# Kernel optimization log

Hardware: AMD Instinct MI355X
Metric: run time of the kernel (lower is better)

The kernel has to match this reference:

```python
import jax, jax.numpy as jnp
import numpy as np

VOCAB, EMBED, HIDDEN, CH = 500, 80, 512, 128
B, L, T = 128, 784, 256


def setup_inputs() -> dict:
    key = jax.random.key(0)
    ks = jax.random.split(key, 14)
    s = lambda fan_in: 1.0 / np.sqrt(fan_in)
    return {
        "latent_rep": jax.random.normal(ks[0], (B, L, CH), jnp.float32),
        "formulas": jax.random.randint(ks[1], (B, T), 0, VOCAB),
        "embedding": jax.random.normal(ks[2], (VOCAB, EMBED), jnp.float32),
        "W_ih": jax.random.uniform(ks[3], (4 * HIDDEN, HIDDEN + EMBED), jnp.float32, -s(HIDDEN), s(HIDDEN)),
        "b_ih": jax.random.uniform(ks[4], (4 * HIDDEN,), jnp.float32, -s(HIDDEN), s(HIDDEN)),
        "W_hh": jax.random.uniform(ks[5], (4 * HIDDEN, HIDDEN), jnp.float32, -s(HIDDEN), s(HIDDEN)),
        "b_hh": jax.random.uniform(ks[6], (4 * HIDDEN,), jnp.float32, -s(HIDDEN), s(HIDDEN)),
        "Wh": jax.random.uniform(ks[7], (HIDDEN, CH), jnp.float32, -s(CH), s(CH)),
        "bh": jax.random.uniform(ks[8], (HIDDEN,), jnp.float32, -s(CH), s(CH)),
        "Wc": jax.random.uniform(ks[9], (HIDDEN, CH), jnp.float32, -s(CH), s(CH)),
        "bc": jax.random.uniform(ks[10], (HIDDEN,), jnp.float32, -s(CH), s(CH)),
        "Wo": jax.random.uniform(ks[11], (HIDDEN, CH), jnp.float32, -s(CH), s(CH)),
        "bo": jax.random.uniform(ks[12], (HIDDEN,), jnp.float32, -s(CH), s(CH)),
    }


def reference(latent_rep, formulas, embedding, W_ih, b_ih, W_hh, b_hh, Wh, bh, Wc, bc, Wo, bo):
    # init_lstm: tanh(Linear(mean over spatial positions))
    mean_lr = latent_rep.mean(axis=1)                       # [B, C]
    h0 = jnp.tanh(mean_lr @ Wh.T + bh)                       # [B, H]
    c0 = jnp.tanh(mean_lr @ Wc.T + bc)
    o0 = jnp.tanh(mean_lr @ Wo.T + bo)                       # fixed across steps in source

    emb = embedding[formulas]                                # [B, T, E]
    xs = jnp.swapaxes(emb, 0, 1)                             # [T, B, E]

    def step(carry, emb_t):
        h, c = carry
        inp = jnp.concatenate([o0, emb_t], axis=1)           # [B, H+E]
        gates = inp @ W_ih.T + b_ih + h @ W_hh.T + b_hh      # [B, 4H]
        i_g, f_g, g_g, o_g = jnp.split(gates, 4, axis=1)
        c_new = jax.nn.sigmoid(f_g) * c + jax.nn.sigmoid(i_g) * jnp.tanh(g_g)
        h_new = jax.nn.sigmoid(o_g) * jnp.tanh(c_new)
        # dropout in eval mode = identity
        return (h_new, c_new), h_new

    _, hs = jax.lax.scan(step, (h0, c0), xs)                 # hs: [T, B, H]
    return jnp.swapaxes(hs, 0, 1)                            # [B, T, H]
```

## Files before the change

kernel.cpp:

```cpp
#include <hip/hip_runtime.h>
#include <hip/hip_bf16.h>
#include <stdint.h>

typedef unsigned int uint32;
typedef __attribute__((ext_vector_type(8))) short short8;
typedef __attribute__((ext_vector_type(4))) float f32x4;

#define NB 128
#define NT 256
#define NH 512
#define NE 80
#define NCH 128
#define NL 784
#define NV 500
#define NG4 2048

__device__ __forceinline__ unsigned short f2bf(float f){
  union { float f; unsigned int i; } v; v.f = f;
  unsigned int r = v.i + 0x7FFFu + ((v.i >> 16) & 1u);
  return (unsigned short)(r >> 16);
}
__device__ __forceinline__ float sigf(float x){ return 1.0f/(1.0f + __expf(-x)); }
__device__ __forceinline__ float tanhfast(float x){ return 1.0f - 2.0f/(__expf(2.0f*x)+1.0f); }

__global__ void k_mean(const float* __restrict__ lat, float* __restrict__ meanv){
  int b = blockIdx.x;
  int tid = threadIdx.x;
  int c4 = tid & 31;
  int part = tid >> 5;
  const float4* row = (const float4*)(lat + (size_t)b*NL*NCH);
  float sx=0.f, sy=0.f, sz=0.f, sw=0.f;
  for (int l=part; l<NL; l+=8){
    float4 v = row[l*32 + c4];
    sx+=v.x; sy+=v.y; sz+=v.z; sw+=v.w;
  }
  __shared__ float red[8][32][4];
  red[part][c4][0]=sx; red[part][c4][1]=sy; red[part][c4][2]=sz; red[part][c4][3]=sw;
  __syncthreads();
  if (part==0){
    float a0=0,a1=0,a2=0,a3=0;
    #pragma unroll
    for (int p=0;p<8;p++){ a0+=red[p][c4][0]; a1+=red[p][c4][1]; a2+=red[p][c4][2]; a3+=red[p][c4][3]; }
    float4 o; o.x=a0*(1.0f/NL); o.y=a1*(1.0f/NL); o.z=a2*(1.0f/NL); o.w=a3*(1.0f/NL);
    ((float4*)meanv)[b*32 + c4] = o;
  }
}

__global__ void k_init(const float* __restrict__ meanv,
    const float* __restrict__ Wh, const float* __restrict__ bh,
    const float* __restrict__ Wc, const float* __restrict__ bc,
    const float* __restrict__ Wo, const float* __restrict__ bo,
    float* __restrict__ c0, float* __restrict__ o0, unsigned short* __restrict__ hbuf0){
  int b = blockIdx.x; int j = threadIdx.x;
  const float* m = meanv + b*NCH;
  const float4* wh = (const float4*)(Wh + (size_t)j*NCH);
  const float4* wc = (const float4*)(Wc + (size_t)j*NCH);
  const float4* wo = (const float4*)(Wo + (size_t)j*NCH);
  float sh=0.f, sc=0.f, so=0.f;
  for (int c=0; c<NCH/4; c++){
    float4 vh = wh[c], vc = wc[c], vo = wo[c];
    float m0=m[c*4], m1=m[c*4+1], m2=m[c*4+2], m3=m[c*4+3];
    sh += m0*vh.x + m1*vh.y + m2*vh.z + m3*vh.w;
    sc += m0*vc.x + m1*vc.y + m2*vc.z + m3*vc.w;
    so += m0*vo.x + m1*vo.y + m2*vo.z + m3*vo.w;
  }
  float h0 = tanhf(sh + bh[j]);
  c0[b*NH+j] = tanhf(sc + bc[j]);
  o0[b*NH+j] = tanhf(so + bo[j]);
  hbuf0[b*NH+j] = f2bf(h0);
}

__global__ void k_table(const float* __restrict__ emb,
                        const float* __restrict__ Wih,
                        float* __restrict__ table){
  int v = blockIdx.x;
  int n = blockIdx.y*256 + threadIdx.x;
  const float4* wr = (const float4*)(Wih + (size_t)n*(NH+NE) + NH);
  const float4* er = (const float4*)(emb + v*NE);
  float s = 0.f;
  for (int e4=0; e4<NE/4; e4++){
    float4 w = wr[e4], e = er[e4];
    s += w.x*e.x + w.y*e.y + w.z*e.z + w.w*e.w;
  }
  table[(size_t)v*NG4 + n] = s;
}

__global__ void k_base(const float* __restrict__ o0,
                       const float* __restrict__ Wih,
                       const float* __restrict__ bih,
                       const float* __restrict__ bhh,
                       float* __restrict__ base){
  int b = blockIdx.x;
  int n = blockIdx.y*256 + threadIdx.x;
  const float4* o = (const float4*)(o0 + b*NH);
  const float4* wr = (const float4*)(Wih + (size_t)n*(NH+NE));
  float s = bih[n] + bhh[n];
  for (int k4=0;k4<NH/4;k4++){
    float4 w = wr[k4], v = o[k4];
    s += w.x*v.x + w.y*v.y + w.z*v.z + w.w*v.w;
  }
  base[(size_t)b*NG4 + n] = s;
}

#define HBUF_U (NB*(NH/2))

__global__ __launch_bounds__(256, 1) void k_lstm(
    const float* __restrict__ Whh,
    const int* __restrict__ formulas,
    const float* __restrict__ table,
    const float* __restrict__ base,
    const float* __restrict__ c0,
    uint32* hbuf, int* flags,
    float* __restrict__ out)
{
  int bid = blockIdx.x;
  int g = bid & 7, s = bid >> 3;
  int tid = threadIdx.x;
  int lane = tid & 63, w = tid >> 6;
  int b0 = g*16, u0 = s*32;

  __shared__ __align__(16) char h_lds[16*1024];
  __shared__ float G[16*132 + 4];

  short8 bw[2][16];
  {
    int krow = (lane >> 4) * 8;
    #pragma unroll
    for (int h2=0; h2<2; h2++){
      int c_loc = w*32 + h2*16 + (lane & 15);
      int wrow = (c_loc >> 5)*NH + u0 + (c_loc & 31);
      const float4* p4 = (const float4*)(Whh + (size_t)wrow*NH + krow);
      #pragma unroll
      for (int ks=0; ks<16; ks++){
        float4 lo = p4[ks*8], hi = p4[ks*8+1];
        short8 t;
        t[0]=(short)f2bf(lo.x); t[1]=(short)f2bf(lo.y); t[2]=(short)f2bf(lo.z); t[3]=(short)f2bf(lo.w);
        t[4]=(short)f2bf(hi.x); t[5]=(short)f2bf(hi.y); t[6]=(short)f2bf(hi.z); t[7]=(short)f2bf(hi.w);
        bw[h2][ks] = t;
      }
    }
  }

  int r_e = tid >> 4, up = tid & 15;
  int be = b0 + r_e;
  float cst0 = c0[be*NH + u0 + 2*up];
  float cst1 = c0[be*NH + u0 + 2*up + 1];

  float2 bsv[4];
  #pragma unroll
  for (int gt=0; gt<4; gt++)
    bsv[gt] = *(const float2*)(base + (size_t)be*NG4 + gt*NH + u0 + 2*up);

  float2 tbv[4];
  {
    int tok0 = formulas[be*NT + 0];
    #pragma unroll
    for (int gt=0; gt<4; gt++)
      tbv[gt] = *(const float2*)(table + (size_t)tok0*NG4 + gt*NH + u0 + 2*up);
  }

  int arow = lane & 15;
  int abyte = arow*1024 + ((lane>>4)*8)*2;
  int aswz = (arow & 7) << 4;

  int* myflag = flags + g*16 + s;
  const int* pollptr = flags + g*16 + (lane & 15);

  for (int t=0; t<NT; t++){
    const uint32* hrd = hbuf + (t & 1)*HBUF_U;
    uint32*       hwr = hbuf + ((t+1) & 1)*HBUF_U;

    if (t > 0){
      if (w == 0){
        int guard = 0;
        while (1){
          int v = __hip_atomic_load(pollptr, __ATOMIC_RELAXED, __HIP_MEMORY_SCOPE_AGENT);
          if (__all(v >= t)) break;
          __builtin_amdgcn_s_sleep(1);
          if (++guard > (1<<16)) break;
        }
      }
      __syncthreads();
    }

    uint32 vals[16];
    #pragma unroll
    for (int it=0; it<16; it++){
      int i = tid + it*256;
      int r = i >> 8, cu = i & 255;
      vals[it] = __hip_atomic_load(&hrd[(b0+r)*(NH/2) + cu],
                                   __ATOMIC_RELAXED, __HIP_MEMORY_SCOPE_AGENT);
    }
    #pragma unroll
    for (int it=0; it<16; it++){
      int i = tid + it*256;
      int r = i >> 8, cu = i & 255;
      *(uint32*)(h_lds + ((r*1024 + cu*4) ^ ((r & 7) << 4))) = vals[it];
    }
    __syncthreads();

    f32x4 acc0 = {0.f,0.f,0.f,0.f}, acc1 = {0.f,0.f,0.f,0.f};
    #pragma unroll
    for (int ks=0; ks<16; ks++){
      short8 a = *(const short8*)(h_lds + ((abyte + ks*64) ^ aswz));
      acc0 = __builtin_amdgcn_mfma_f32_16x16x32_bf16(a, bw[0][ks], acc0, 0, 0, 0);
      acc1 = __builtin_amdgcn_mfma_f32_16x16x32_bf16(a, bw[1][ks], acc1, 0, 0, 0);
    }

    {
      int rbase = (lane>>4)*4;
      int col0 = (w*2+0)*16 + (lane&15);
      int col1 = (w*2+1)*16 + (lane&15);
      #pragma unroll
      for (int r4=0;r4<4;r4++){
        G[(rbase+r4)*132 + col0] = acc0[r4];
        G[(rbase+r4)*132 + col1] = acc1[r4];
      }
    }
    __syncthreads();

    float hn0, hn1;
    {
      const float* Gr = G + r_e*132 + 2*up;
      float gi0 = Gr[0]   + tbv[0].x + bsv[0].x;
      float gi1 = Gr[1]   + tbv[0].y + bsv[0].y;
      float gf0 = Gr[32]  + tbv[1].x + bsv[1].x;
      float gf1 = Gr[33]  + tbv[1].y + bsv[1].y;
      float gg0 = Gr[64]  + tbv[2].x + bsv[2].x;
      float gg1 = Gr[65]  + tbv[2].y + bsv[2].y;
      float go0 = Gr[96]  + tbv[3].x + bsv[3].x;
      float go1 = Gr[97]  + tbv[3].y + bsv[3].y;
      float cn0 = sigf(gf0)*cst0 + sigf(gi0)*tanhfast(gg0);
      float cn1 = sigf(gf1)*cst1 + sigf(gi1)*tanhfast(gg1);
      cst0 = cn0; cst1 = cn1;
      hn0 = sigf(go0)*tanhfast(cn0);
      hn1 = sigf(go1)*tanhfast(cn1);
    }

    if (t < NT-1){
      uint32 packed = (uint32)f2bf(hn0) | ((uint32)f2bf(hn1) << 16);
      __hip_atomic_store(&hwr[be*(NH/2) + (u0/2 + up)], packed,
                         __ATOMIC_RELAXED, __HIP_MEMORY_SCOPE_AGENT);
    }
    __syncthreads();
    if (t < NT-1 && tid == 0)
      __hip_atomic_store(myflag, t+1, __ATOMIC_RELAXED, __HIP_MEMORY_SCOPE_AGENT);

    {
      float2 ov; ov.x = hn0; ov.y = hn1;
      *(float2*)(out + ((size_t)be*NT + t)*NH + u0 + 2*up) = ov;
    }
    if (t < NT-1){
      int tokn = formulas[be*NT + t + 1];
      #pragma unroll
      for (int gt=0; gt<4; gt++)
        tbv[gt] = *(const float2*)(table + (size_t)tokn*NG4 + gt*NH + u0 + 2*up);
    }
  }
}

extern "C" void kernel_launch(void* const* d_in, const int* in_sizes, int n_in,
                              void* d_out, int out_size, void* d_ws, size_t ws_size,
                              hipStream_t stream) {
  const float* lat      = (const float*)d_in[0];
  const int*   formulas = (const int*)d_in[1];
  const float* emb      = (const float*)d_in[2];
  const float* Wih      = (const float*)d_in[3];
  const float* bih      = (const float*)d_in[4];
  const float* Whh      = (const float*)d_in[5];
  const float* bhh      = (const float*)d_in[6];
  const float* Wh       = (const float*)d_in[7];
  const float* bh       = (const float*)d_in[8];
  const float* Wc       = (const float*)d_in[9];
  const float* bc       = (const float*)d_in[10];
  const float* Wo       = (const float*)d_in[11];
  const float* bo       = (const float*)d_in[12];
  float* out = (float*)d_out;

  char* ws = (char*)d_ws;
  float* meanv = (float*)ws;  ws += (size_t)NB*NCH*4;
  float* c0    = (float*)ws;  ws += (size_t)NB*NH*4;
  float* o0    = (float*)ws;  ws += (size_t)NB*NH*4;
  float* table = (float*)ws;  ws += (size_t)NV*NG4*4;
  float* base  = (float*)ws;  ws += (size_t)NB*NG4*4;
  uint32* hbuf = (uint32*)ws; ws += (size_t)2*HBUF_U*4;
  int*   flags = (int*)ws;    ws += 512;

  hipMemsetAsync(flags, 0, 512, stream);
  k_mean <<<NB, 256, 0, stream>>>(lat, meanv);
  k_init <<<NB, NH, 0, stream>>>(meanv, Wh, bh, Wc, bc, Wo, bo, c0, o0, (unsigned short*)hbuf);
  k_table<<<dim3(NV, 8), 256, 0, stream>>>(emb, Wih, table);
  k_base <<<dim3(NB, 8), 256, 0, stream>>>(o0, Wih, bih, bhh, base);
  k_lstm <<<NB, 256, 0, stream>>>(Whh, formulas, table, base, c0, hbuf, flags, out);
}
```

Before: 712.6 us.

## Fuse mean/init kernels, retile table and base GEMVs, drop LSTM poll barrier

Merges the spatial mean and LSTM-initialisation kernels into one launch. The embedding-projection table and the o0 base-gate kernels are rewritten to stage operands in LDS and reuse weights held in registers. In the recurrent kernel, every wave now polls the step flags itself, replacing the single-wave poll followed by a block barrier. These changes target launch overhead, redundant global weight reads in the precompute stage, and per-step barrier latency. The trade-off is more atomic polling traffic, and the table kernel now runs only 32 blocks.

```diff
diff --git a/kernel.cpp b/kernel.cpp
--- a/kernel.cpp
+++ b/kernel.cpp
@@ -3,6 +3,7 @@
 #include <stdint.h>
 
 typedef unsigned int uint32;
+typedef unsigned long long uint64;
 typedef __attribute__((ext_vector_type(8))) short short8;
 typedef __attribute__((ext_vector_type(4))) float f32x4;
 
@@ -15,6 +16,8 @@
 #define NV 500
 #define NG4 2048
 
+#define HBUF_U (NB*(NH/2))
+
 __device__ __forceinline__ unsigned short f2bf(float f){
   union { float f; unsigned int i; } v; v.f = f;
   unsigned int r = v.i + 0x7FFFu + ((v.i >> 16) & 1u);
@@ -23,86 +26,123 @@
 __device__ __forceinline__ float sigf(float x){ return 1.0f/(1.0f + __expf(-x)); }
 __device__ __forceinline__ float tanhfast(float x){ return 1.0f - 2.0f/(__expf(2.0f*x)+1.0f); }
 
-__global__ void k_mean(const float* __restrict__ lat, float* __restrict__ meanv){
-  int b = blockIdx.x;
-  int tid = threadIdx.x;
-  int c4 = tid & 31;
-  int part = tid >> 5;
-  const float4* row = (const float4*)(lat + (size_t)b*NL*NCH);
-  float sx=0.f, sy=0.f, sz=0.f, sw=0.f;
-  for (int l=part; l<NL; l+=8){
-    float4 v = row[l*32 + c4];
-    sx+=v.x; sy+=v.y; sz+=v.z; sw+=v.w;
-  }
-  __shared__ float red[8][32][4];
-  red[part][c4][0]=sx; red[part][c4][1]=sy; red[part][c4][2]=sz; red[part][c4][3]=sw;
-  __syncthreads();
-  if (part==0){
-    float a0=0,a1=0,a2=0,a3=0;
-    #pragma unroll
-    for (int p=0;p<8;p++){ a0+=red[p][c4][0]; a1+=red[p][c4][1]; a2+=red[p][c4][2]; a3+=red[p][c4][3]; }
-    float4 o; o.x=a0*(1.0f/NL); o.y=a1*(1.0f/NL); o.z=a2*(1.0f/NL); o.w=a3*(1.0f/NL);
-    ((float4*)meanv)[b*32 + c4] = o;
-  }
-}
-
-__global__ void k_init(const float* __restrict__ meanv,
+__global__ __launch_bounds__(512) void k_meaninit(const float* __restrict__ lat,
     const float* __restrict__ Wh, const float* __restrict__ bh,
     const float* __restrict__ Wc, const float* __restrict__ bc,
     const float* __restrict__ Wo, const float* __restrict__ bo,
-    float* __restrict__ c0, float* __restrict__ o0, unsigned short* __restrict__ hbuf0){
-  int b = blockIdx.x; int j = threadIdx.x;
-  const float* m = meanv + b*NCH;
+    float* __restrict__ c0, float* __restrict__ o0, uint32* __restrict__ hbuf0){
+  int b = blockIdx.x;
+  int tid = threadIdx.x;
+  __shared__ float red[16][32][4];
+  __shared__ float msh[128];
+  __shared__ unsigned short hsh[NH];
+
+  {
+    int c4 = tid & 31, part = tid >> 5;
+    const float4* row = (const float4*)(lat + (size_t)b*NL*NCH);
+    float sx=0.f, sy=0.f, sz=0.f, sw=0.f;
+    for (int l=part; l<NL; l+=16){
+      float4 v = row[l*32 + c4];
+      sx+=v.x; sy+=v.y; sz+=v.z; sw+=v.w;
+    }
+    red[part][c4][0]=sx; red[part][c4][1]=sy; red[part][c4][2]=sz; red[part][c4][3]=sw;
+  }
+  __syncthreads();
+  if (tid < 128){
+    int cc4 = tid >> 2, ci = tid & 3;
+    float a = 0.f;
+    #pragma unroll
+    for (int p=0;p<16;p++) a += red[p][cc4][ci];
+    msh[tid] = a * (1.0f/NL);
+  }
+  __syncthreads();
+
+  int j = tid;
   const float4* wh = (const float4*)(Wh + (size_t)j*NCH);
   const float4* wc = (const float4*)(Wc + (size_t)j*NCH);
   const float4* wo = (const float4*)(Wo + (size_t)j*NCH);
   float sh=0.f, sc=0.f, so=0.f;
+  #pragma unroll 8
   for (int c=0; c<NCH/4; c++){
     float4 vh = wh[c], vc = wc[c], vo = wo[c];
-    float m0=m[c*4], m1=m[c*4+1], m2=m[c*4+2], m3=m[c*4+3];
-    sh += m0*vh.x + m1*vh.y + m2*vh.z + m3*vh.w;
-    sc += m0*vc.x + m1*vc.y + m2*vc.z + m3*vc.w;
-    so += m0*vo.x + m1*vo.y + m2*vo.z + m3*vo.w;
+    float4 mv = *(const float4*)&msh[c*4];
+    sh += mv.x*vh.x + mv.y*vh.y + mv.z*vh.z + mv.w*vh.w;
+    sc += mv.x*vc.x + mv.y*vc.y + mv.z*vc.z + mv.w*vc.w;
+    so += mv.x*vo.x + mv.y*vo.y + mv.z*vo.z + mv.w*vo.w;
   }
   float h0 = tanhf(sh + bh[j]);
   c0[b*NH+j] = tanhf(sc + bc[j]);
   o0[b*NH+j] = tanhf(so + bo[j]);
-  hbuf0[b*NH+j] = f2bf(h0);
-}
-
-__global__ void k_table(const float* __restrict__ emb,
-                        const float* __restrict__ Wih,
-                        float* __restrict__ table){
-  int v = blockIdx.x;
-  int n = blockIdx.y*256 + threadIdx.x;
-  const float4* wr = (const float4*)(Wih + (size_t)n*(NH+NE) + NH);
-  const float4* er = (const float4*)(emb + v*NE);
-  float s = 0.f;
-  for (int e4=0; e4<NE/4; e4++){
-    float4 w = wr[e4], e = er[e4];
-    s += w.x*e.x + w.y*e.y + w.z*e.z + w.w*e.w;
-  }
-  table[(size_t)v*NG4 + n] = s;
-}
-
-__global__ void k_base(const float* __restrict__ o0,
+  hsh[j] = f2bf(h0);
+  __syncthreads();
+  if (j < NH/2)
+    hbuf0[(size_t)b*(NH/2) + j] = (uint32)hsh[2*j] | ((uint32)hsh[2*j+1] << 16);
+}
+
+__global__ __launch_bounds__(256) void k_table(const float* __restrict__ emb,
+                                               const float* __restrict__ Wih,
+                                               float* __restrict__ table){
+  int n0 = blockIdx.x * 64;
+  int tid = threadIdx.x;
+  __shared__ float el[100][84];
+  int n = tid & 63;
+  float4 wr[20];
+  {
+    const float4* wp = (const float4*)(Wih + (size_t)(n0+n)*(NH+NE) + NH);
+    #pragma unroll
+    for (int k=0;k<20;k++) wr[k] = wp[k];
+  }
+  for (int v0 = 0; v0 < NV; v0 += 100){
+    __syncthreads();
+    for (int i = tid; i < 100*20; i += 256){
+      int r = i/20, k4 = i - r*20;
+      *(float4*)&el[r][k4*4] = *(const float4*)(emb + (size_t)(v0+r)*NE + k4*4);
+    }
+    __syncthreads();
+    int vl = tid >> 6;
+    for (int v = vl; v < 100; v += 4){
+      float s = 0.f;
+      #pragma unroll
+      for (int k=0;k<20;k++){
+        float4 e = *(const float4*)&el[v][k*4];
+        s += e.x*wr[k].x + e.y*wr[k].y + e.z*wr[k].z + e.w*wr[k].w;
+      }
+      table[(size_t)(v0+v)*NG4 + n0 + n] = s;
+    }
+  }
+}
+
+__global__ __launch_bounds__(256) void k_base(const float* __restrict__ o0,
                        const float* __restrict__ Wih,
                        const float* __restrict__ bih,
                        const float* __restrict__ bhh,
                        float* __restrict__ base){
-  int b = blockIdx.x;
-  int n = blockIdx.y*256 + threadIdx.x;
-  const float4* o = (const float4*)(o0 + b*NH);
-  const float4* wr = (const float4*)(Wih + (size_t)n*(NH+NE));
-  float s = bih[n] + bhh[n];
-  for (int k4=0;k4<NH/4;k4++){
-    float4 w = wr[k4], v = o[k4];
-    s += w.x*v.x + w.y*v.y + w.z*v.z + w.w*v.w;
-  }
-  base[(size_t)b*NG4 + n] = s;
-}
-
-#define HBUF_U (NB*(NH/2))
+  int bg = blockIdx.x & 7, nc = blockIdx.x >> 3;
+  int b0 = bg*16, n0 = nc*128;
+  int tid = threadIdx.x;
+  __shared__ float ol[16][520];
+  for (int i = tid; i < 16*128; i += 256){
+    int r = i >> 7, k4 = i & 127;
+    *(float4*)&ol[r][k4*4] = *(const float4*)(o0 + (size_t)(b0+r)*NH + k4*4);
+  }
+  __syncthreads();
+  int r = tid >> 4;
+  int ni = (tid & 15)*8;
+  float acc[8];
+  #pragma unroll
+  for (int q=0;q<8;q++) acc[q] = bih[n0+ni+q] + bhh[n0+ni+q];
+  for (int k4 = 0; k4 < 128; k4++){
+    float4 ov = *(const float4*)&ol[r][k4*4];
+    #pragma unroll
+    for (int q=0;q<8;q++){
+      float4 wv = *(const float4*)(Wih + (size_t)(n0+ni+q)*(NH+NE) + k4*4);
+      acc[q] += ov.x*wv.x + ov.y*wv.y + ov.z*wv.z + ov.w*wv.w;
+    }
+  }
+  #pragma unroll
+  for (int q=0;q<8;q++)
+    base[(size_t)(b0+r)*NG4 + n0+ni+q] = acc[q];
+}
 
 __global__ __launch_bounds__(256, 1) void k_lstm(
     const float* __restrict__ Whh,
@@ -171,16 +211,13 @@
     uint32*       hwr = hbuf + ((t+1) & 1)*HBUF_U;
 
     if (t > 0){
-      if (w == 0){
-        int guard = 0;
-        while (1){
-          int v = __hip_atomic_load(pollptr, __ATOMIC_RELAXED, __HIP_MEMORY_SCOPE_AGENT);
-          if (__all(v >= t)) break;
-          __builtin_amdgcn_s_sleep(1);
-          if (++guard > (1<<16)) break;
-        }
+      int guard = 0;
+      while (1){
+        int v = __hip_atomic_load(pollptr, __ATOMIC_RELAXED, __HIP_MEMORY_SCOPE_AGENT);
+        if (__all(v >= t)) break;
+        __builtin_amdgcn_s_sleep(1);
+        if (++guard > (1<<16)) break;
       }
-      __syncthreads();
     }
 
     uint32 vals[16];
@@ -239,7 +276,7 @@
 
     if (t < NT-1){
       uint32 packed = (uint32)f2bf(hn0) | ((uint32)f2bf(hn1) << 16);
-      __hip_atomic_store(&hwr[be*(NH/2) + (u0/2 + up)], packed,
+      __hip_atomic_store(&hwr[(size_t)be*(NH/2) + (u0/2 + up)], packed,
                          __ATOMIC_RELAXED, __HIP_MEMORY_SCOPE_AGENT);
     }
     __syncthreads();
@@ -278,7 +315,6 @@
   float* out = (float*)d_out;
 
   char* ws = (char*)d_ws;
-  float* meanv = (float*)ws;  ws += (size_t)NB*NCH*4;
   float* c0    = (float*)ws;  ws += (size_t)NB*NH*4;
   float* o0    = (float*)ws;  ws += (size_t)NB*NH*4;
   float* table = (float*)ws;  ws += (size_t)NV*NG4*4;
@@ -287,9 +323,8 @@
   int*   flags = (int*)ws;    ws += 512;
 
   hipMemsetAsync(flags, 0, 512, stream);
-  k_mean <<<NB, 256, 0, stream>>>(lat, meanv);
-  k_init <<<NB, NH, 0, stream>>>(meanv, Wh, bh, Wc, bc, Wo, bo, c0, o0, (unsigned short*)hbuf);
-  k_table<<<dim3(NV, 8), 256, 0, stream>>>(emb, Wih, table);
-  k_base <<<dim3(NB, 8), 256, 0, stream>>>(o0, Wih, bih, bhh, base);
-  k_lstm <<<NB, 256, 0, stream>>>(Whh, formulas, table, base, c0, hbuf, flags, out);
-}
+  k_meaninit<<<NB, 512, 0, stream>>>(lat, Wh, bh, Wc, bc, Wo, bo, c0, o0, hbuf);
+  k_table  <<<32, 256, 0, stream>>>(emb, Wih, table);
+  k_base   <<<NB, 256, 0, stream>>>(o0, Wih, bih, bhh, base);
+  k_lstm   <<<NB, 256, 0, stream>>>(Whh, formulas, table, base, c0, hbuf, flags, out);
+}
```

Measured after the change: 846.9 us. +18.8%, slower.
